# Optimization experiments

Hardware: AMD Instinct MI355X
Metric: run time of the kernel (lower is better)

The kernel has to match this reference:

```python
import jax, jax.numpy as jnp
import numpy as np

V, S, D, H, DK, DV, DFF, L, B, PAD = 32000, 2048, 512, 8, 64, 64, 2048, 2, 2, 0


def _pos_encoding(s, d):
    pos = jnp.arange(s, dtype=jnp.float32)[:, None]
    idx = jnp.arange(d // 2, dtype=jnp.float32)
    ang = pos / (10000.0 ** (2.0 * idx / d))  # [s, d/2]
    pe = jnp.zeros((s, d), jnp.float32)
    pe = pe.at[:, 0::2].set(jnp.sin(ang))
    pe = pe.at[:, 1::2].set(jnp.cos(ang))
    return pe


def _stable_softmax(x):
    # matches torch: max clamped to >= 0, denom + 1e-9 (all -inf row -> zeros)
    m = jnp.clip(jnp.max(x, axis=-1, keepdims=True), 0.0, None)
    e = jnp.exp(x - m)
    return e / (jnp.sum(e, axis=-1, keepdims=True) + 1e-9)


def _ln(x, s, b):
    mu = jnp.mean(x, axis=-1, keepdims=True)
    var = jnp.mean((x - mu) ** 2, axis=-1, keepdims=True)
    return (x - mu) / jnp.sqrt(var + 1e-5) * s + b


def setup_inputs() -> dict:
    key = jax.random.key(0)
    ks = jax.random.split(key, 16)
    sc = 0.02
    emb = sc * jax.random.normal(ks[1], (V, D), jnp.float32)
    emb = emb.at[PAD].set(0.0)  # padding_idx row is zero
    return {
        'x': jax.random.randint(ks[0], (B, S), 0, V),
        'padding_mask': jnp.zeros((B, S), bool),
        'emb': emb,
        'wq': sc * jax.random.normal(ks[2], (L, D, H * DK), jnp.float32),
        'wk': sc * jax.random.normal(ks[3], (L, D, H * DK), jnp.float32),
        'wv': sc * jax.random.normal(ks[4], (L, D, H * DV), jnp.float32),
        'wo': sc * jax.random.normal(ks[5], (L, H * DV, D), jnp.float32),
        'ln1_s': jnp.ones((L, D), jnp.float32),
        'ln1_b': jnp.zeros((L, D), jnp.float32),
        'ln2_s': jnp.ones((L, D), jnp.float32),
        'ln2_b': jnp.zeros((L, D), jnp.float32),
        'w1': sc * jax.random.normal(ks[6], (L, D, DFF), jnp.float32),
        'b1': jnp.zeros((L, DFF), jnp.float32),
        'w2': sc * jax.random.normal(ks[7], (L, DFF, D), jnp.float32),
        'b2': jnp.zeros((L, D), jnp.float32),
        'w_out': sc * jax.random.normal(ks[8], (D, V), jnp.float32),
    }


def _forward(x, padding_mask, emb, wq, wk, wv, wo, ln1_s, ln1_b, ln2_s, ln2_b, w1, b1, w2, b2, w_out):
    b, s = x.shape
    pe = _pos_encoding(s, D)[None]  # [1, s, D]
    pe = jnp.where(padding_mask[:, :, None], 0.0, pe)  # zero PE at padding tokens
    h = emb[x] + pe  # [b, s, D]
    # causal mask INCLUDES the diagonal (torch.triu default), union with padding rows/cols
    causal = jnp.triu(jnp.ones((s, s), bool))
    mask = causal[None, None] | padding_mask[:, None, None, :] | padding_mask[:, None, :, None]
    for l in range(L):
        q = (h @ wq[l]).reshape(b, s, H, DK).transpose(0, 2, 1, 3)
        k = (h @ wk[l]).reshape(b, s, H, DK).transpose(0, 2, 1, 3)
        v = (h @ wv[l]).reshape(b, s, H, DV).transpose(0, 2, 1, 3)
        scores = jnp.einsum('bhqd,bhkd->bhqk', q, k) / jnp.sqrt(jnp.float32(DK))
        scores = jnp.where(mask, -jnp.inf, scores)
        attn = _stable_softmax(scores)  # [b, H, s, s]
        o = jnp.einsum('bhqk,bhkd->bhqd', attn, v)
        o = o.transpose(0, 2, 1, 3).reshape(b, s, H * DV) @ wo[l]
        h = _ln(h + o, ln1_s[l], ln1_b[l])  # post-LN residual
        ff = jax.nn.gelu(h @ w1[l] + b1[l], approximate=False) @ w2[l] + b2[l]
        h = _ln(h + ff, ln2_s[l], ln2_b[l])
    return h @ w_out  # logits [b, s, V]


def reference(x, padding_mask, emb, wq, wk, wv, wo, ln1_s, ln1_b, ln2_s, ln2_b, w1, b1, w2, b2, w_out):
    return _forward(x, padding_mask, emb, wq, wk, wv, wo, ln1_s, ln1_b, ln2_s, ln2_b, w1, b1, w2, b2, w_out)
```

## Files before the change

### kernel.cpp

```cpp
#include <hip/hip_runtime.h>
#include <hip/hip_bf16.h>
#include <stdint.h>

#define VOCAB  32000
#define SLEN   2048
#define DMODEL 512
#define NHEAD  8
#define HDIM   64
#define DFFN   2048
#define NLAYER 2
#define BATCH  2
#define NTOK   (BATCH*SLEN)

typedef unsigned short u16;
using short8 = __attribute__((ext_vector_type(8))) short;
using f32x4  = __attribute__((ext_vector_type(4))) float;
using f32x16 = __attribute__((ext_vector_type(16))) float;
using ushort4v = __attribute__((ext_vector_type(4))) unsigned short;

__device__ __forceinline__ u16 f2bf(float f) {
  union { float f; uint32_t i; } v; v.f = f;
  uint32_t r = v.i + 0x7fffu + ((v.i >> 16) & 1u);
  return (u16)(r >> 16);
}

__device__ __forceinline__ void gload_lds16(const void* g, void* l) {
  __builtin_amdgcn_global_load_lds(
      (const __attribute__((address_space(1))) unsigned int*)g,
      (__attribute__((address_space(3))) unsigned int*)l,
      16, 0, 0);
}

__device__ __forceinline__ void tr_tile(float (*t)[33],
                                        const float* __restrict__ in, u16* __restrict__ out,
                                        int K, int N, int nb, int kb, int tid) {
  int tx = tid & 31, ty = tid >> 5;
  #pragma unroll
  for (int i = 0; i < 32; i += 8)
    t[ty + i][tx] = in[(size_t)(kb + ty + i) * N + nb + tx];
  __syncthreads();
  #pragma unroll
  for (int i = 0; i < 32; i += 8)
    out[(size_t)(nb + ty + i) * K + kb + tx] = f2bf(t[tx][ty + i]);
}

__global__ void transpose_all(const float* __restrict__ wq, const float* __restrict__ wk,
                              const float* __restrict__ wv, const float* __restrict__ wo,
                              const float* __restrict__ w1, const float* __restrict__ w2,
                              const float* __restrict__ wout,
                              u16* __restrict__ qkvT, u16* __restrict__ woT,
                              u16* __restrict__ w1T, u16* __restrict__ w2T,
                              u16* __restrict__ woutK) {
  __shared__ float t[32][33];
  const int bid = blockIdx.x;
  const int tid = threadIdx.x;
  if (bid < 2048) {
    int job = bid >> 8, tile = bid & 255;
    int l = job >> 2, which = job & 3;
    const float* in = (which == 0) ? wq : (which == 1) ? wk : (which == 2) ? wv : wo;
    in += (size_t)l * DMODEL * DMODEL;
    u16* out = (which < 3) ? qkvT + (size_t)l * 1536 * DMODEL + (size_t)which * DMODEL * DMODEL
                           : woT + (size_t)l * DMODEL * DMODEL;
    tr_tile(t, in, out, DMODEL, DMODEL, (tile & 15) * 32, (tile >> 4) * 32, tid);
  } else if (bid < 6144) {
    int rel = bid - 2048;
    int job = rel >> 10, tile = rel & 1023;
    int l = job >> 1, which = job & 1;
    const float* in; u16* out; int K, N;
    if (which == 0) { in = w1 + (size_t)l * DMODEL * DFFN; out = w1T + (size_t)l * DFFN * DMODEL; K = DMODEL; N = DFFN; }
    else            { in = w2 + (size_t)l * DFFN * DMODEL; out = w2T + (size_t)l * DMODEL * DFFN; K = DFFN; N = DMODEL; }
    int ntx = N / 32;
    tr_tile(t, in, out, K, N, (tile % ntx) * 32, (tile / ntx) * 32, tid);
  } else {
    int rel = bid - 6144;
    int nb = rel >> 3, kt = rel & 7;
    u16* dst = woutK + ((size_t)(nb * 8 + kt)) * 16384;
    #pragma unroll
    for (int kg = 0; kg < 8; ++kg) {
      short8 v;
      #pragma unroll
      for (int e = 0; e < 8; ++e)
        v[e] = (short)f2bf(wout[(size_t)(kt * 64 + kg * 8 + e) * VOCAB + nb * 256 + tid]);
      *(short8*)(dst + (kg * 256 + tid) * 8) = v;
    }
  }
}

__global__ void embed_pe(const int* __restrict__ x, const float* __restrict__ emb,
                         float* __restrict__ hf, u16* __restrict__ hb) {
  int tok = blockIdx.x;
  int s = tok & (SLEN - 1);
  int d = threadIdx.x << 2;
  int t = x[tok];
  float4 ev = *(const float4*)(emb + (size_t)t * DMODEL + d);
  float pos = (float)s;
  const float cexp = -0.03597789207803197f;
  float i0 = (float)(d >> 1);
  float a0 = pos * expf(cexp * i0);
  float a1 = pos * expf(cexp * (i0 + 1.0f));
  float h0 = ev.x + sinf(a0);
  float h1 = ev.y + cosf(a0);
  float h2 = ev.z + sinf(a1);
  float h3 = ev.w + cosf(a1);
  size_t o = (size_t)tok * DMODEL + d;
  *(float4*)(hf + o) = make_float4(h0, h1, h2, h3);
  hb[o + 0] = f2bf(h0); hb[o + 1] = f2bf(h1);
  hb[o + 2] = f2bf(h2); hb[o + 3] = f2bf(h3);
}

template<int EPI>
__global__ __launch_bounds__(256, 3)
void gemm_r64(const u16* __restrict__ A, const u16* __restrict__ Bt,
              float* __restrict__ Cf, u16* __restrict__ Cb, u16* __restrict__ Vt,
              const float* __restrict__ bias, int M, int N, int K) {
  __shared__ u16 lds[3 * 8192];
  const int tid = threadIdx.x;
  const int lane = tid & 63;
  const int lr = lane & 15, lg = lane >> 4;
  const int sx = lr & 7;
  const int w = tid >> 6;
  const int wm = (w >> 1) * 32;
  const int wn = (w & 1) * 32;

  const int nwg = gridDim.x * gridDim.y;
  const int bid = blockIdx.y * gridDim.x + blockIdx.x;
  const int g  = (bid & 7) * (nwg >> 3) + (bid >> 3);
  const int bx = g % (int)gridDim.x;
  const int by = g / (int)gridDim.x;
  const int m0 = by * 64, n0 = bx * 64;
  const int NT = K >> 6;

  auto stage = [&](int slot, int t) {
    u16* ab = lds + slot * 8192;
    const u16* Ag = A + (size_t)m0 * K + t * 64;
    #pragma unroll
    for (int i = 0; i < 2; ++i) {
      int cl = i * 256 + tid;
      int row = cl >> 3, c = cl & 7;
      gload_lds16(Ag + (size_t)row * K + ((c ^ (row & 7)) << 3), ab + cl * 8);
    }
    u16* bb = ab + 4096;
    const u16* Bg = Bt + (size_t)n0 * K + t * 64;
    #pragma unroll
    for (int i = 0; i < 2; ++i) {
      int cl = i * 256 + tid;
      int row = cl >> 3, c = cl & 7;
      gload_lds16(Bg + (size_t)row * K + ((c ^ (row & 7)) << 3), bb + cl * 8);
    }
  };

  f32x4 acc[2][2] = {};
  stage(0, 0); stage(1, 1); stage(2, 2);

  for (int t = 0; t < NT; ++t) {
    const u16* ab = lds + (t % 3) * 8192;
    const u16* bb = ab + 4096;
    if (t < NT - 2)       asm volatile("s_waitcnt vmcnt(8)" ::: "memory");
    else if (t == NT - 2) asm volatile("s_waitcnt vmcnt(4)" ::: "memory");
    else                  asm volatile("s_waitcnt vmcnt(0)" ::: "memory");
    __builtin_amdgcn_s_barrier();
    __builtin_amdgcn_sched_barrier(0);

    short8 af[4], bf[4];
    #pragma unroll
    for (int mi = 0; mi < 2; ++mi)
      #pragma unroll
      for (int ks = 0; ks < 2; ++ks)
        af[mi * 2 + ks] = *(const short8*)(ab + (wm + mi * 16 + lr) * 64 + ((((ks << 2) + lg) ^ sx) << 3));
    #pragma unroll
    for (int ni = 0; ni < 2; ++ni)
      #pragma unroll
      for (int ks = 0; ks < 2; ++ks)
        bf[ni * 2 + ks] = *(const short8*)(bb + (wn + ni * 16 + lr) * 64 + ((((ks << 2) + lg) ^ sx) << 3));
    asm volatile("s_waitcnt lgkmcnt(0)" ::: "memory");
    __builtin_amdgcn_sched_barrier(0);
    __builtin_amdgcn_s_setprio(1);
    #pragma unroll
    for (int ks = 0; ks < 2; ++ks)
      #pragma unroll
      for (int mi = 0; mi < 2; ++mi)
        #pragma unroll
        for (int ni = 0; ni < 2; ++ni)
          acc[mi][ni] = __builtin_amdgcn_mfma_f32_16x16x32_bf16(af[mi * 2 + ks], bf[ni * 2 + ks], acc[mi][ni], 0, 0, 0);
    __builtin_amdgcn_s_setprio(0);
    __builtin_amdgcn_s_barrier();
    __builtin_amdgcn_sched_barrier(0);
    if (t + 3 < NT) stage(t % 3, t + 3);
  }

  #pragma unroll
  for (int mi = 0; mi < 2; ++mi)
    #pragma unroll
    for (int ni = 0; ni < 2; ++ni) {
      const int col = n0 + wn + ni * 16 + lr;
      const int row0 = m0 + wm + mi * 16 + lg * 4;
      float bv = 0.f;
      if constexpr (EPI == 3) bv = bias[col];
      if constexpr (EPI == 2) {
        if (col >= 1024) {
          int hd = col - 1024, hh = hd >> 6, d = hd & 63;
          int b2 = row0 >> 11, s = row0 & (SLEN - 1);
          int c2 = (s >> 3) & 15, e2 = s & 7;
          int cs2 = c2 ^ (d & 7);
          ushort4v pk;
          #pragma unroll
          for (int j = 0; j < 4; ++j) pk[j] = f2bf(acc[mi][ni][j]);
          size_t va = ((size_t)((b2 * NHEAD + hh) * HDIM + d) << 11) + (s & ~127) + cs2 * 8 + e2;
          *(ushort4v*)(Vt + va) = pk;
          continue;
        }
      }
      #pragma unroll
      for (int j = 0; j < 4; ++j) {
        const int row = row0 + j;
        float v = acc[mi][ni][j];
        if constexpr (EPI == 0) {
          Cf[(size_t)row * N + col] = v;
        } else if constexpr (EPI == 2) {
          int dh = col & 63;
          int cs = (col & ~63) | ((((dh >> 3) ^ (row & 7)) << 3) | (dh & 7));
          Cb[(size_t)row * N + cs] = f2bf(v);
        } else {
          float xb = v + bv;
          Cb[(size_t)row * N + col] = f2bf(0.5f * xb * (1.0f + erff(xb * 0.7071067811865476f)));
        }
      }
    }
}

__global__ __launch_bounds__(512, 2)
void gemm8(const u16* __restrict__ A, const u16* __restrict__ Bkt,
           float* __restrict__ Cf, int M, int N, int K) {
  __shared__ u16 lds[65536];
  const int tid = threadIdx.x;
  const int lane = tid & 63;
  const int l31 = lane & 31, l5 = lane >> 5;
  const int rx = lane & 7;
  const int w = tid >> 6;
  const int wm = (w >> 2) * 64;
  const int wn = (w & 3) * 64;
  const int nwg = gridDim.x * gridDim.y;
  const int bid = blockIdx.y * gridDim.x + blockIdx.x;
  const int g  = (bid & 7) * (nwg >> 3) + (bid >> 3);
  const int bx = g / (int)gridDim.y;
  const int by = g % (int)gridDim.y;
  const int m0 = by * 256, n0 = bx * 256;
  const int NT = K >> 6;

  auto stageA = [&](int t, int mh) {
    u16* dst = lds + (t & 1) * 32768 + mh * 8192;
    const u16* src = A + (size_t)(m0 + mh * 128) * K + t * 64;
    #pragma unroll
    for (int i = 0; i < 2; ++i) {
      int c = i * 512 + tid;
      int row = c >> 3, cc = c & 7;
      gload_lds16(src + (size_t)row * K + ((cc ^ (row & 7)) << 3), dst + c * 8);
    }
  };
  auto stageB = [&](int t, int kk) {
    u16* dst = lds + (t & 1) * 32768 + 16384 + kk * 8192;
    const u16* src = Bkt + ((size_t)bx * NT + t) * 16384 + kk * 8192;
    #pragma unroll
    for (int i = 0; i < 2; ++i) {
      int c = i * 512 + tid;
      gload_lds16(src + c * 8, dst + c * 8);
    }
  };

  f32x16 accL[2][2] = {};
  f32x16 accH[2][2] = {};

  stageA(0, 0); stageA(0, 1); stageB(0, 0); stageB(0, 1);

  for (int t = 0; t < NT; ++t) {
    const u16* Ab = lds + (t & 1) * 32768;
    const u16* Bb = Ab + 16384;
    const bool pf = (t + 1 < NT);
    short8 af[4], b0[4], b1[4];

    asm volatile("s_waitcnt vmcnt(2)" ::: "memory");
    __builtin_amdgcn_s_barrier();
    __builtin_amdgcn_sched_barrier(0);
    #pragma unroll
    for (int mf = 0; mf < 2; ++mf)
      #pragma unroll
      for (int ks = 0; ks < 2; ++ks)
        af[mf * 2 + ks] = *(const short8*)(Ab + (wm + mf * 32 + l31) * 64 + (((ks * 2 + l5) ^ rx) << 3));
    #pragma unroll
    for (int nf = 0; nf < 2; ++nf)
      #pragma unroll
      for (int ks = 0; ks < 2; ++ks)
        b0[nf * 2 + ks] = *(const short8*)(Bb + ((ks * 2 + l5) * 256 + wn + nf * 32 + l31) * 8);
    if (pf) stageA(t + 1, 0);
    __builtin_amdgcn_sched_barrier(0);
    __builtin_amdgcn_s_setprio(1);
    #pragma unroll
    for (int ks = 0; ks < 2; ++ks)
      #pragma unroll
      for (int mf = 0; mf < 2; ++mf)
        #pragma unroll
        for (int nf = 0; nf < 2; ++nf)
          accL[mf][nf] = __builtin_amdgcn_mfma_f32_32x32x16_bf16(af[mf * 2 + ks], b0[nf * 2 + ks], accL[mf][nf], 0, 0, 0);
    __builtin_amdgcn_s_setprio(0);

    #pragma unroll
    for (int mf = 0; mf < 2; ++mf)
      #pragma unroll
      for (int ks = 0; ks < 2; ++ks)
        af[mf * 2 + ks] = *(const short8*)(Ab + 8192 + (wm + mf * 32 + l31) * 64 + (((ks * 2 + l5) ^ rx) << 3));
    if (pf) stageA(t + 1, 1);
    __builtin_amdgcn_sched_barrier(0);
    __builtin_amdgcn_s_setprio(1);
    #pragma unroll
    for (int ks = 0; ks < 2; ++ks)
      #pragma unroll
      for (int mf = 0; mf < 2; ++mf)
        #pragma unroll
        for (int nf = 0; nf < 2; ++nf)
          accH[mf][nf] = __builtin_amdgcn_mfma_f32_32x32x16_bf16(af[mf * 2 + ks], b0[nf * 2 + ks], accH[mf][nf], 0, 0, 0);
    __builtin_amdgcn_s_setprio(0);

    if (pf) { asm volatile("s_waitcnt vmcnt(4)" ::: "memory"); }
    else    { asm volatile("s_waitcnt vmcnt(0)" ::: "memory"); }
    __builtin_amdgcn_s_barrier();
    __builtin_amdgcn_sched_barrier(0);
    #pragma unroll
    for (int mf = 0; mf < 2; ++mf)
      #pragma unroll
      for (int ks = 0; ks < 2; ++ks)
        af[mf * 2 + ks] = *(const short8*)(Ab + (wm + mf * 32 + l31) * 64 + (((4 + ks * 2 + l5) ^ rx) << 3));
    #pragma unroll
    for (int nf = 0; nf < 2; ++nf)
      #pragma unroll
      for (int ks = 0; ks < 2; ++ks)
        b1[nf * 2 + ks] = *(const short8*)(Bb + ((4 + ks * 2 + l5) * 256 + wn + nf * 32 + l31) * 8);
    if (pf) stageB(t + 1, 0);
    __builtin_amdgcn_sched_barrier(0);
    __builtin_amdgcn_s_setprio(1);
    #pragma unroll
    for (int ks = 0; ks < 2; ++ks)
      #pragma unroll
      for (int mf = 0; mf < 2; ++mf)
        #pragma unroll
        for (int nf = 0; nf < 2; ++nf)
          accL[mf][nf] = __builtin_amdgcn_mfma_f32_32x32x16_bf16(af[mf * 2 + ks], b1[nf * 2 + ks], accL[mf][nf], 0, 0, 0);
    __builtin_amdgcn_s_setprio(0);

    #pragma unroll
    for (int mf = 0; mf < 2; ++mf)
      #pragma unroll
      for (int ks = 0; ks < 2; ++ks)
        af[mf * 2 + ks] = *(const short8*)(Ab + 8192 + (wm + mf * 32 + l31) * 64 + (((4 + ks * 2 + l5) ^ rx) << 3));
    if (pf) stageB(t + 1, 1);
    __builtin_amdgcn_sched_barrier(0);
    __builtin_amdgcn_s_setprio(1);
    #pragma unroll
    for (int ks = 0; ks < 2; ++ks)
      #pragma unroll
      for (int mf = 0; mf < 2; ++mf)
        #pragma unroll
        for (int nf = 0; nf < 2; ++nf)
          accH[mf][nf] = __builtin_amdgcn_mfma_f32_32x32x16_bf16(af[mf * 2 + ks], b1[nf * 2 + ks], accH[mf][nf], 0, 0, 0);
    __builtin_amdgcn_s_setprio(0);
  }

  #pragma unroll
  for (int mh = 0; mh < 2; ++mh)
    #pragma unroll
    for (int mf = 0; mf < 2; ++mf)
      #pragma unroll
      for (int nf = 0; nf < 2; ++nf) {
        const int col = n0 + wn + nf * 32 + l31;
        const int rbase = m0 + mh * 128 + wm + mf * 32 + 4 * l5;
        #pragma unroll
        for (int reg = 0; reg < 16; ++reg) {
          const int row = rbase + (reg & 3) + 8 * (reg >> 2);
          float v = mh ? accH[mf][nf][reg] : accL[mf][nf][reg];
          __builtin_nontemporal_store(v, &Cf[(size_t)row * N + col]);
        }
      }
}

__global__ __launch_bounds__(256, 2)
void flash_attn(const u16* __restrict__ qkv, const u16* __restrict__ vT,
                u16* __restrict__ Og) {
  const int bid = blockIdx.x;
  const int qt = (bid < 256) ? (31 - (bid >> 4)) : ((bid - 256) >> 4);
  const int hb = bid & 15;
  const int h  = hb & 7;
  const int b  = hb >> 3;
  const int tid = threadIdx.x;
  const int lane = tid & 63;
  const int w = tid >> 6;
  const int lr = lane & 15, lg = lane >> 4;
  const int sx = lr & 7;

  __shared__ u16 Ks[128 * 64];
  __shared__ u16 Vs[64 * 128];
  __shared__ u16 Pl[4][16 * 132];

  const u16* Qb = qkv + (size_t)(b * SLEN + qt * 64) * 1536 + h * 64;
  const u16* Kb = qkv + (size_t)(b * SLEN) * 1536 + 512 + h * 64;
  const u16* Vb = vT + ((size_t)(b * NHEAD + h) * HDIM) * SLEN;

  #pragma unroll
  for (int r = 0; r < 2; ++r) {
    int chunk = r * 256 + tid;
    int row = chunk >> 3, cc = chunk & 7;
    gload_lds16(Qb + (size_t)row * 1536 + cc * 8, Ks + chunk * 8);
  }
  __syncthreads();
  short8 qf[2];
  #pragma unroll
  for (int ks = 0; ks < 2; ++ks)
    qf[ks] = *(const short8*)(Ks + (w * 16 + lr) * 64 + ((((ks << 2) + lg) ^ sx) << 3));
  __syncthreads();

  f32x4 mrow = {};
  f32x4 lrow = {};
  f32x4 accO[4] = {};
  const float SC = 0.18033688011112042f;

  const int ktmax = (qt * 64 + 62) >> 7;
  for (int kt = 0; kt <= ktmax; ++kt) {
    #pragma unroll
    for (int r = 0; r < 4; ++r) {
      int chunk = r * 256 + tid;
      int row = chunk >> 3, cc = chunk & 7;
      gload_lds16(Kb + (size_t)(kt * 128 + row) * 1536 + cc * 8, Ks + chunk * 8);
    }
    #pragma unroll
    for (int r = 0; r < 4; ++r) {
      int chunk = r * 256 + tid;
      int drow = chunk >> 4, cc = chunk & 15;
      gload_lds16(Vb + (size_t)drow * SLEN + kt * 128 + cc * 8, Vs + chunk * 8);
    }
    asm volatile("s_waitcnt vmcnt(4)" ::: "memory");
    __builtin_amdgcn_s_barrier();
    __builtin_amdgcn_sched_barrier(0);

    f32x4 sfr[8];
    #pragma unroll
    for (int ni = 0; ni < 8; ++ni) {
      f32x4 a = {};
      #pragma unroll
      for (int ks = 0; ks < 2; ++ks) {
        short8 kf = *(const short8*)(Ks + (ni * 16 + lr) * 64 + ((((ks << 2) + lg) ^ sx) << 3));
        a = __builtin_amdgcn_mfma_f32_16x16x32_bf16(qf[ks], kf, a, 0, 0, 0);
      }
      sfr[ni] = a * SC;
    }
    if (kt == ktmax) {
      #pragma unroll
      for (int ni = 0; ni < 8; ++ni)
        #pragma unroll
        for (int j = 0; j < 4; ++j) {
          int kg = kt * 128 + ni * 16 + lr;
          int qg = qt * 64 + w * 16 + lg * 4 + j;
          if (kg >= qg) sfr[ni][j] = -1e30f;
        }
    }
    f32x4 tmax = sfr[0];
    #pragma unroll
    for (int ni = 1; ni < 8; ++ni)
      #pragma unroll
      for (int j = 0; j < 4; ++j) tmax[j] = fmaxf(tmax[j], sfr[ni][j]);
    #pragma unroll
    for (int off = 1; off < 16; off <<= 1)
      #pragma unroll
      for (int j = 0; j < 4; ++j) tmax[j] = fmaxf(tmax[j], __shfl_xor(tmax[j], off));
    f32x4 mnew, scl;
    #pragma unroll
    for (int j = 0; j < 4; ++j) {
      mnew[j] = fmaxf(mrow[j], tmax[j]);
      scl[j]  = exp2f(mrow[j] - mnew[j]);
    }
    f32x4 rsum = {};
    #pragma unroll
    for (int ni = 0; ni < 8; ++ni)
      #pragma unroll
      for (int j = 0; j < 4; ++j) {
        float pv = exp2f(sfr[ni][j] - mnew[j]);
        sfr[ni][j] = pv;
        rsum[j] += pv;
      }
    #pragma unroll
    for (int off = 1; off < 16; off <<= 1)
      #pragma unroll
      for (int j = 0; j < 4; ++j) rsum[j] += __shfl_xor(rsum[j], off);
    #pragma unroll
    for (int j = 0; j < 4; ++j) { lrow[j] = lrow[j] * scl[j] + rsum[j]; mrow[j] = mnew[j]; }
    #pragma unroll
    for (int di = 0; di < 4; ++di)
      #pragma unroll
      for (int j = 0; j < 4; ++j) accO[di][j] *= scl[j];

    u16* pw = Pl[w];
    #pragma unroll
    for (int ni = 0; ni < 8; ++ni)
      #pragma unroll
      for (int j = 0; j < 4; ++j)
        pw[(lg * 4 + j) * 132 + ni * 16 + lr] = f2bf(sfr[ni][j]);

    asm volatile("s_waitcnt lgkmcnt(0)" ::: "memory");
    asm volatile("s_waitcnt vmcnt(0)" ::: "memory");
    __builtin_amdgcn_s_barrier();
    __builtin_amdgcn_sched_barrier(0);

    #pragma unroll
    for (int ks = 0; ks < 4; ++ks) {
      short8 pa = *(const short8*)(pw + lr * 132 + ks * 32 + lg * 8);
      #pragma unroll
      for (int di = 0; di < 4; ++di) {
        short8 vbf = *(const short8*)(Vs + (di * 16 + lr) * 128 + ((((ks << 2) + lg) ^ sx) << 3));
        accO[di] = __builtin_amdgcn_mfma_f32_16x16x32_bf16(pa, vbf, accO[di], 0, 0, 0);
      }
    }
    __syncthreads();
  }

  u16* Ob = Og + ((size_t)(b * SLEN + qt * 64 + w * 16)) * DMODEL + h * HDIM;
  f32x4 inv;
  #pragma unroll
  for (int j = 0; j < 4; ++j) inv[j] = 1.0f / (lrow[j] + 1e-9f);
  #pragma unroll
  for (int di = 0; di < 4; ++di)
    #pragma unroll
    for (int j = 0; j < 4; ++j)
      Ob[(size_t)(lg * 4 + j) * DMODEL + di * 16 + lr] = f2bf(accO[di][j] * inv[j]);
}

__global__ void ln_res(const float* __restrict__ hin, const float* __restrict__ yin,
                       const float* __restrict__ badd,
                       const float* __restrict__ sc, const float* __restrict__ bi,
                       float* __restrict__ hout, u16* __restrict__ hb) {
  int row = blockIdx.x * 4 + (threadIdx.x >> 6);
  int lane = threadIdx.x & 63;
  size_t base = (size_t)row * DMODEL;
  float v[8];
  float sum = 0.f;
  #pragma unroll
  for (int i = 0; i < 8; ++i) {
    int d = lane * 8 + i;
    float t = hin[base + d] + yin[base + d];
    if (badd) t += badd[d];
    v[i] = t; sum += t;
  }
  #pragma unroll
  for (int off = 1; off < 64; off <<= 1) sum += __shfl_xor(sum, off);
  float mu = sum * (1.f / 512.f);
  float sq = 0.f;
  #pragma unroll
  for (int i = 0; i < 8; ++i) { float dv = v[i] - mu; sq += dv * dv; }
  #pragma unroll
  for (int off = 1; off < 64; off <<= 1) sq += __shfl_xor(sq, off);
  float rstd = rsqrtf(sq * (1.f / 512.f) + 1e-5f);
  #pragma unroll
  for (int i = 0; i < 8; ++i) {
    int d = lane * 8 + i;
    float o = (v[i] - mu) * rstd * sc[d] + bi[d];
    hout[base + d] = o;
    hb[base + d] = f2bf(o);
  }
}

extern "C" void kernel_launch(void* const* d_in, const int* in_sizes, int n_in,
                              void* d_out, int out_size, void* d_ws, size_t ws_size,
                              hipStream_t stream) {
  (void)in_sizes; (void)n_in; (void)out_size; (void)ws_size;
  const int*   x    = (const int*)d_in[0];
  const float* emb  = (const float*)d_in[2];
  const float* wq   = (const float*)d_in[3];
  const float* wk   = (const float*)d_in[4];
  const float* wv   = (const float*)d_in[5];
  const float* wo   = (const float*)d_in[6];
  const float* ln1s = (const float*)d_in[7];
  const float* ln1b = (const float*)d_in[8];
  const float* ln2s = (const float*)d_in[9];
  const float* ln2b = (const float*)d_in[10];
  const float* w1   = (const float*)d_in[11];
  const float* b1   = (const float*)d_in[12];
  const float* w2   = (const float*)d_in[13];
  const float* b2   = (const float*)d_in[14];
  const float* wout = (const float*)d_in[15];

  char* p = (char*)d_ws;
  auto alloc = [&](size_t bytes) { char* q = p; p += (bytes + 255) & ~(size_t)255; return q; };
  float* hf    = (float*)alloc((size_t)NTOK * DMODEL * 4);
  u16*  hb     = (u16*) alloc((size_t)NTOK * DMODEL * 2);
  u16*  qkvb   = (u16*) alloc((size_t)NTOK * 1536 * 2);
  u16*  vTb    = (u16*) alloc((size_t)NTOK * DMODEL * 2);
  u16*  obuf   = (u16*) alloc((size_t)NTOK * DMODEL * 2);
  float* y32   = (float*)alloc((size_t)NTOK * DMODEL * 4);
  u16*  ff1g   = (u16*) alloc((size_t)NTOK * DFFN * 2);
  u16*  wqkvT  = (u16*) alloc((size_t)NLAYER * 1536 * DMODEL * 2);
  u16*  woT    = (u16*) alloc((size_t)NLAYER * DMODEL * DMODEL * 2);
  u16*  w1T    = (u16*) alloc((size_t)NLAYER * DMODEL * DFFN * 2);
  u16*  w2T    = (u16*) alloc((size_t)NLAYER * DFFN * DMODEL * 2);
  u16*  woutK  = (u16*) alloc((size_t)VOCAB * DMODEL * 2);

  transpose_all<<<dim3(7144), 256, 0, stream>>>(wq, wk, wv, wo, w1, w2, wout,
                                                wqkvT, woT, w1T, w2T, woutK);

  embed_pe<<<NTOK, 128, 0, stream>>>(x, emb, hf, hb);

  for (int l = 0; l < NLAYER; ++l) {
    size_t o = (size_t)l * DMODEL * DMODEL;
    gemm_r64<2><<<dim3(24, 64), 256, 0, stream>>>(
        hb, wqkvT + (size_t)l * 1536 * DMODEL, nullptr, qkvb, vTb, nullptr, NTOK, 1536, DMODEL);
    flash_attn<<<dim3(512), 256, 0, stream>>>(qkvb, vTb, obuf);
    gemm_r64<0><<<dim3(8, 64), 256, 0, stream>>>(
        obuf, woT + o, y32, nullptr, nullptr, nullptr, NTOK, DMODEL, DMODEL);
    ln_res<<<NTOK / 4, 256, 0, stream>>>(hf, y32, nullptr, ln1s + l * DMODEL, ln1b + l * DMODEL, hf, hb);
    gemm_r64<3><<<dim3(32, 64), 256, 0, stream>>>(
        hb, w1T + (size_t)l * DFFN * DMODEL, nullptr, ff1g, nullptr, b1 + l * DFFN, NTOK, DFFN, DMODEL);
    gemm_r64<0><<<dim3(8, 64), 256, 0, stream>>>(
        ff1g, w2T + (size_t)l * DMODEL * DFFN, y32, nullptr, nullptr, nullptr, NTOK, DMODEL, DFFN);
    ln_res<<<NTOK / 4, 256, 0, stream>>>(hf, y32, b2 + l * DMODEL, ln2s + l * DMODEL, ln2b + l * DMODEL, hf, hb);
  }
  gemm8<<<dim3(VOCAB / 256, NTOK / 256), 512, 0, stream>>>(
      hb, woutK, (float*)d_out, NTOK, VOCAB, DMODEL);
}
```

Measured before the change: 480.0 us.

## Double-buffer K tiles in flash attention to prefetch next tile

Adds a second LDS buffer for K so the next key tile is prefetched while the current tile's QK^T and PV run, adjusting vmcnt waits to count the outstanding prefetch loads. The goal is to hide global-to-LDS latency of K loads behind compute. It adds 16KB of LDS per block, which may reduce occupancy under launch_bounds(256,2), and relies on careful vmcnt counting for correctness.

```diff
diff --git a/kernel.cpp b/kernel.cpp
--- a/kernel.cpp
+++ b/kernel.cpp
@@ -395,7 +395,7 @@
   const int lr = lane & 15, lg = lane >> 4;
   const int sx = lr & 7;
 
-  __shared__ u16 Ks[128 * 64];
+  __shared__ u16 Ks[2][128 * 64];
   __shared__ u16 Vs[64 * 128];
   __shared__ u16 Pl[4][16 * 132];
 
@@ -403,41 +403,54 @@
   const u16* Kb = qkv + (size_t)(b * SLEN) * 1536 + 512 + h * 64;
   const u16* Vb = vT + ((size_t)(b * NHEAD + h) * HDIM) * SLEN;
 
+  const int ktmax = (qt * 64 + 62) >> 7;
+
+  auto stageK = [&](int t) {
+    u16* kd = Ks[t & 1];
+    #pragma unroll
+    for (int r = 0; r < 4; ++r) {
+      int chunk = r * 256 + tid;
+      int row = chunk >> 3, cc = chunk & 7;
+      gload_lds16(Kb + (size_t)(t * 128 + row) * 1536 + cc * 8, kd + chunk * 8);
+    }
+  };
+  auto stageV = [&](int t) {
+    #pragma unroll
+    for (int r = 0; r < 4; ++r) {
+      int chunk = r * 256 + tid;
+      int drow = chunk >> 4, cc = chunk & 15;
+      gload_lds16(Vb + (size_t)drow * SLEN + t * 128 + cc * 8, Vs + chunk * 8);
+    }
+  };
+
   #pragma unroll
   for (int r = 0; r < 2; ++r) {
     int chunk = r * 256 + tid;
     int row = chunk >> 3, cc = chunk & 7;
-    gload_lds16(Qb + (size_t)row * 1536 + cc * 8, Ks + chunk * 8);
+    gload_lds16(Qb + (size_t)row * 1536 + cc * 8, Ks[0] + chunk * 8);
   }
   __syncthreads();
   short8 qf[2];
   #pragma unroll
   for (int ks = 0; ks < 2; ++ks)
-    qf[ks] = *(const short8*)(Ks + (w * 16 + lr) * 64 + ((((ks << 2) + lg) ^ sx) << 3));
+    qf[ks] = *(const short8*)(Ks[0] + (w * 16 + lr) * 64 + ((((ks << 2) + lg) ^ sx) << 3));
   __syncthreads();
+
+  stageK(0);
 
   f32x4 mrow = {};
   f32x4 lrow = {};
   f32x4 accO[4] = {};
   const float SC = 0.18033688011112042f;
 
-  const int ktmax = (qt * 64 + 62) >> 7;
   for (int kt = 0; kt <= ktmax; ++kt) {
-    #pragma unroll
-    for (int r = 0; r < 4; ++r) {
-      int chunk = r * 256 + tid;
-      int row = chunk >> 3, cc = chunk & 7;
-      gload_lds16(Kb + (size_t)(kt * 128 + row) * 1536 + cc * 8, Ks + chunk * 8);
-    }
-    #pragma unroll
-    for (int r = 0; r < 4; ++r) {
-      int chunk = r * 256 + tid;
-      int drow = chunk >> 4, cc = chunk & 15;
-      gload_lds16(Vb + (size_t)drow * SLEN + kt * 128 + cc * 8, Vs + chunk * 8);
-    }
-    asm volatile("s_waitcnt vmcnt(4)" ::: "memory");
+    stageV(kt);
+    if (kt + 1 <= ktmax) stageK(kt + 1);
+    if (kt + 1 <= ktmax) { asm volatile("s_waitcnt vmcnt(8)" ::: "memory"); }
+    else                 { asm volatile("s_waitcnt vmcnt(4)" ::: "memory"); }
     __builtin_amdgcn_s_barrier();
     __builtin_amdgcn_sched_barrier(0);
+    const u16* kb = Ks[kt & 1];
 
     f32x4 sfr[8];
     #pragma unroll
@@ -445,7 +458,7 @@
       f32x4 a = {};
       #pragma unroll
       for (int ks = 0; ks < 2; ++ks) {
-        short8 kf = *(const short8*)(Ks + (ni * 16 + lr) * 64 + ((((ks << 2) + lg) ^ sx) << 3));
+        short8 kf = *(const short8*)(kb + (ni * 16 + lr) * 64 + ((((ks << 2) + lg) ^ sx) << 3));
         a = __builtin_amdgcn_mfma_f32_16x16x32_bf16(qf[ks], kf, a, 0, 0, 0);
       }
       sfr[ni] = a * SC;
@@ -503,7 +516,8 @@
         pw[(lg * 4 + j) * 132 + ni * 16 + lr] = f2bf(sfr[ni][j]);
 
     asm volatile("s_waitcnt lgkmcnt(0)" ::: "memory");
-    asm volatile("s_waitcnt vmcnt(0)" ::: "memory");
+    if (kt + 1 <= ktmax) { asm volatile("s_waitcnt vmcnt(4)" ::: "memory"); }
+    else                 { asm volatile("s_waitcnt vmcnt(0)" ::: "memory"); }
     __builtin_amdgcn_s_barrier();
     __builtin_amdgcn_sched_barrier(0);
 
@@ -516,7 +530,8 @@
         accO[di] = __builtin_amdgcn_mfma_f32_16x16x32_bf16(pa, vbf, accO[di], 0, 0, 0);
       }
     }
-    __syncthreads();
+    __builtin_amdgcn_s_barrier();
+    __builtin_amdgcn_sched_barrier(0);
   }
 
   u16* Ob = Og + ((size_t)(b * SLEN + qt * 64 + w * 16)) * DMODEL + h * HDIM;
```

After: 473.7 us. About the same (-1.3%).
